# Kernel tuning notes

Measured on AMD Instinct MI355X. Metric: run time of the kernel, lower is better.

The kernel has to match this reference:

```python
import jax, jax.numpy as jnp
import numpy as np
from jax.scipy.ndimage import map_coordinates

B, H, W, C = 131072, 12, 12, 1

def setup_inputs() -> dict:
    key = jax.random.key(0)
    ks = jax.random.split(key, 9)
    s = 0.05
    return {
        "x":   jax.random.normal(ks[0], (B, H, W, C), jnp.float32),
        "k1":  jax.random.normal(ks[1], (7, 7, C, 8), jnp.float32) * s,
        "bc1": jnp.zeros((8,), jnp.float32),
        "k2":  jax.random.normal(ks[2], (5, 5, 8, 10), jnp.float32) * s,
        "bc2": jnp.zeros((10,), jnp.float32),
        "W1":  jax.random.normal(ks[3], (90, 32), jnp.float32) * s,
        "b1":  jnp.zeros((32,), jnp.float32),
        "W2":  jax.random.normal(ks[4], (32, 6), jnp.float32) * s,
        "b2":  jnp.array([1.0, 0.0, 0.0, 0.0, 1.0, 0.0], jnp.float32),  # near-identity transform
    }

def _conv(x, k, b):
    y = jax.lax.conv_general_dilated(x, k, window_strides=(1, 1), padding='SAME',
                                     dimension_numbers=('NHWC', 'HWIO', 'NHWC'))
    return y + b

def _maxpool2(x):
    return jax.lax.reduce_window(x, -jnp.inf, jax.lax.max,
                                 (1, 2, 2, 1), (1, 2, 2, 1), 'VALID')

def _forward(x, k1, bc1, k2, bc2, W1, b1, W2, b2):
    # localization network
    xs = jax.nn.relu(_maxpool2(_conv(x, k1, bc1)))     # (B,6,6,8)
    xs = jax.nn.relu(_maxpool2(_conv(xs, k2, bc2)))    # (B,3,3,10)
    b = x.shape[0]
    xs = xs.reshape(b, 90)
    theta = jax.nn.relu(xs @ W1 + b1) @ W2 + b2        # (B,6)
    # grid = inv((1+1e-5)*I2) @ theta  ==  theta / (1+1e-5)
    theta = (theta / (1.0 + 1e-5)).reshape(b, 2, 3)
    h, w = x.shape[1], x.shape[2]
    # target grid in normalized [-1,1] coords
    yn, xn = jnp.meshgrid(jnp.linspace(-1.0, 1.0, h), jnp.linspace(-1.0, 1.0, w), indexing='ij')
    tgt = jnp.stack([xn, yn, jnp.ones_like(xn)], 0).reshape(3, -1)  # (3, H*W)
    src = jnp.einsum('bij,jk->bik', theta, tgt)        # (B,2,H*W): (x_src, y_src)
    px = (src[:, 0] + 1.0) * (w - 1) * 0.5             # pixel coords
    py = (src[:, 1] + 1.0) * (h - 1) * 0.5
    coords = jnp.stack([py.reshape(b, h, w), px.reshape(b, h, w)], 1)  # (B,2,H,W)
    def sample_one(img, coord):  # img (H,W,C), coord (2,H,W)
        return jax.vmap(
            lambda ch: map_coordinates(ch, [coord[0], coord[1]], order=1, mode='reflect'),
            in_axes=2, out_axes=2)(img)
    return jax.vmap(sample_one)(x, coords)             # (B,H,W,C)

def reference(x, k1, bc1, k2, bc2, W1, b1, W2, b2):
    return _forward(x, k1, bc1, k2, bc2, W1, b1, W2, b2)
```

## Files before the change

### kernel.cpp

```cpp
#include <hip/hip_runtime.h>

typedef __attribute__((ext_vector_type(8))) short bfrag;
typedef __attribute__((ext_vector_type(4))) float facc;

__device__ __forceinline__ short f2bf(float f) {
    unsigned u = __float_as_uint(f);
    u += 0x7FFFu + ((u >> 16) & 1u);
    return (short)(u >> 16);
}
__device__ __forceinline__ int refl12(int i) {
    int r = i % 24; if (r < 0) r += 24; return (r < 12) ? r : 23 - r;
}
__device__ __forceinline__ facc mfma16(bfrag a, bfrag b, facc c) {
    return __builtin_amdgcn_mfma_f32_16x16x32_bf16(a, b, c, 0, 0, 0);
}

#define WB1_E 0
#define WB2_E 184320
#define W1T_E 350208
#define W2T_E 353280

#define XS1_STRIDE 296

__global__ void k0_build(const float* __restrict__ k1w, const float* __restrict__ k2w,
                         const float* __restrict__ W1, const float* __restrict__ W2,
                         short* __restrict__ ws)
{
    const int NW1 = 1152 * 160, NW2 = 576 * 288, NT1 = 32 * 96, NT2 = 16 * 32;
    const int total = NW1 + NW2 + NT1 + NT2;
    for (int q = blockIdx.x * blockDim.x + threadIdx.x; q < total;
         q += gridDim.x * blockDim.x) {
        float val = 0.f;
        short* dst;
        if (q < NW1) {
            int n = q / 160, kk = q - n * 160;
            dst = ws + WB1_E + q;
            int p1 = n >> 5, r = n & 31;
            int hy = (r >> 4) & 1, hx = (r >> 3) & 1, c = r & 7;
            int yp = p1 / 6, xp = p1 - yp * 6;
            int y = 2 * yp + hy, xo = 2 * xp + hx;
            if (kk < 144) {
                int yi = kk / 12, xi = kk - yi * 12;
                int ky = yi - y + 3, kx = xi - xo + 3;
                if (ky >= 0 && ky < 7 && kx >= 0 && kx < 7)
                    val = k1w[(ky * 7 + kx) * 8 + c];
            }
        } else if (q < NW1 + NW2) {
            int qq = q - NW1;
            int n = qq / 288, k2 = qq - n * 288;
            dst = ws + WB2_E + qq;
            int q2 = n >> 6, r = n & 63, g = r >> 4, c2 = r & 15;
            int gy = g >> 1, gx = g & 1;
            int qy = q2 / 3, qx = q2 - qy * 3;
            int Y = 2 * qy + gy, X = 2 * qx + gx;
            int p1 = k2 >> 3, c1 = k2 & 7;
            int yp = p1 / 6, xp = p1 - yp * 6;
            int ky = yp - Y + 2, kx = xp - X + 2;
            if (c2 < 10 && ky >= 0 && ky < 5 && kx >= 0 && kx < 5)
                val = k2w[((ky * 5 + kx) * 8 + c1) * 10 + c2];
        } else if (q < NW1 + NW2 + NT1) {
            int qq = q - NW1 - NW2;
            int j = qq / 96, k = qq - j * 96;
            dst = ws + W1T_E + qq;
            if (k < 90) val = W1[k * 32 + j];
        } else {
            int qq = q - NW1 - NW2 - NT1;
            int t = qq / 32, k = qq - t * 32;
            dst = ws + W2T_E + qq;
            if (t < 6) val = W2[k * 6 + t];
        }
        *dst = f2bf(val);
    }
}

__global__ __launch_bounds__(512) void k12_gemm(
    const float* __restrict__ x, const short* __restrict__ wb1,
    const short* __restrict__ wb2, const short* __restrict__ w1t,
    const short* __restrict__ w2t, const float* __restrict__ bc1,
    const float* __restrict__ bc2, const float* __restrict__ b1,
    const float* __restrict__ b2, float* __restrict__ theta, int B)
{
    __shared__ short xs1L[128 * XS1_STRIDE];
    __shared__ short XS2[128 * 128];
    __shared__ short FC1[128 * 64];

    const int tid = threadIdx.x;
    const int l = tid & 63, w = tid >> 6;
    const int mg = w >> 2, ng = w & 3;
    const int lr = l & 15, lg = l >> 4;
    const long long blkbase = (long long)blockIdx.x * 128;
    const int mloc = mg * 64;

    for (int q = tid; q < 2048; q += 512) {
        bfrag z = {0, 0, 0, 0, 0, 0, 0, 0};
        *(bfrag*)&XS2[q * 8] = z;
    }

    bfrag a[4][5];
    #pragma unroll
    for (int ms = 0; ms < 4; ++ms) {
        long long img = blkbase + mloc + ms * 16 + lr;
        if (img >= B) img = B - 1;
        const float* row = x + (size_t)img * 144;
        #pragma unroll
        for (int t = 0; t < 5; ++t) {
            const int k = t * 32 + lg * 8;
            bfrag f = {0, 0, 0, 0, 0, 0, 0, 0};
            if (k < 144) {
                float4 u0 = *(const float4*)(row + k);
                float4 u1 = *(const float4*)(row + k + 4);
                f[0] = f2bf(u0.x); f[1] = f2bf(u0.y);
                f[2] = f2bf(u0.z); f[3] = f2bf(u0.w);
                f[4] = f2bf(u1.x); f[5] = f2bf(u1.y);
                f[6] = f2bf(u1.z); f[7] = f2bf(u1.w);
            }
            a[ms][t] = f;
        }
    }
    const float bcv = bc1[l & 7];

    auto loadB1 = [&](bfrag (&bb)[2][5], int p1v) {
        const short* p = wb1 + (size_t)(p1v * 32 + lr) * 160 + lg * 8;
        #pragma unroll
        for (int nt = 0; nt < 2; ++nt)
            #pragma unroll
            for (int t = 0; t < 5; ++t)
                bb[nt][t] = *(const bfrag*)(p + (size_t)nt * 16 * 160 + t * 32);
    };
    auto compute1 = [&](bfrag (&bb)[2][5], int p1v) {
        facc acc[4][2];
        #pragma unroll
        for (int ms = 0; ms < 4; ++ms)
            #pragma unroll
            for (int nt = 0; nt < 2; ++nt)
                acc[ms][nt] = (facc){0.f, 0.f, 0.f, 0.f};
        #pragma unroll
        for (int t = 0; t < 5; ++t)
            #pragma unroll
            for (int nt = 0; nt < 2; ++nt)
                #pragma unroll
                for (int ms = 0; ms < 4; ++ms)
                    acc[ms][nt] = mfma16(a[ms][t], bb[nt][t], acc[ms][nt]);
        #pragma unroll
        for (int ms = 0; ms < 4; ++ms)
            #pragma unroll
            for (int i = 0; i < 4; ++i) {
                float p = fmaxf(acc[ms][0][i], acc[ms][1][i]);
                p = fmaxf(p, __shfl_xor(p, 8));
                p = fmaxf(p + bcv, 0.f);
                if ((l & 15) < 8) {
                    int mi = mloc + ms * 16 + lg * 4 + i;
                    xs1L[mi * XS1_STRIDE + p1v * 8 + (l & 7)] = f2bf(p);
                }
            }
    };

    {
        bfrag c0[2][5], c1[2][5];
        loadB1(c0, ng);
        #pragma unroll 1
        for (int jp = 0; jp < 4; ++jp) {
            loadB1(c1, (2 * jp + 1) * 4 + ng);
            compute1(c0, (2 * jp) * 4 + ng);
            loadB1(c0, (2 * jp + 2) * 4 + ng);
            compute1(c1, (2 * jp + 1) * 4 + ng);
        }
        compute1(c0, 32 + ng);
    }
    __syncthreads();

    const int c2 = lr;
    const float bcv2 = (c2 < 10) ? bc2[c2] : 0.f;

    auto loadB2 = [&](bfrag (&bb)[4], int q2v, int tv) {
        #pragma unroll
        for (int g = 0; g < 4; ++g)
            bb[g] = *(const bfrag*)(
                wb2 + (size_t)(q2v * 64 + g * 16 + lr) * 288 + tv * 32 + lg * 8);
    };

    {
        const int q2 = w;
        facc acc[8][4];
        #pragma unroll
        for (int ms = 0; ms < 8; ++ms)
            #pragma unroll
            for (int g = 0; g < 4; ++g)
                acc[ms][g] = (facc){0.f, 0.f, 0.f, 0.f};

        auto mstep8 = [&](bfrag (&bb)[4], int tv) {
            bfrag av[8];
            #pragma unroll
            for (int ms = 0; ms < 8; ++ms) {
                int m = ms * 16 + lr;
                av[ms] = *(const bfrag*)&xs1L[m * XS1_STRIDE + tv * 32 + lg * 8];
            }
            __builtin_amdgcn_s_setprio(1);
            #pragma unroll
            for (int g = 0; g < 4; ++g)
                #pragma unroll
                for (int ms = 0; ms < 8; ++ms)
                    acc[ms][g] = mfma16(av[ms], bb[g], acc[ms][g]);
            __builtin_amdgcn_s_setprio(0);
        };

        bfrag d0[4], d1[4];
        loadB2(d0, q2, 0);
        #pragma unroll 1
        for (int tp = 0; tp < 4; ++tp) {
            loadB2(d1, q2, 2 * tp + 1);
            mstep8(d0, 2 * tp);
            loadB2(d0, q2, 2 * tp + 2);
            mstep8(d1, 2 * tp + 1);
        }
        mstep8(d0, 8);

        #pragma unroll
        for (int ms = 0; ms < 8; ++ms)
            #pragma unroll
            for (int i = 0; i < 4; ++i) {
                float v = fmaxf(fmaxf(acc[ms][0][i], acc[ms][1][i]),
                                fmaxf(acc[ms][2][i], acc[ms][3][i]));
                v = fmaxf(v + bcv2, 0.f);
                if (c2 < 10) {
                    int mi = ms * 16 + lg * 4 + i;
                    int k = q2 * 10 + c2;
                    XS2[mi * 128 + (((k >> 3) ^ (mi & 7)) << 3) + (k & 7)] = f2bf(v);
                }
            }
    }

    if (w < 2) {
        const int q2 = 8;
        const int mBase = w * 64;
        facc acc[4][4];
        #pragma unroll
        for (int ms = 0; ms < 4; ++ms)
            #pragma unroll
            for (int g = 0; g < 4; ++g)
                acc[ms][g] = (facc){0.f, 0.f, 0.f, 0.f};

        auto mstep4 = [&](bfrag (&bb)[4], int tv) {
            bfrag av[4];
            #pragma unroll
            for (int ms = 0; ms < 4; ++ms) {
                int m = mBase + ms * 16 + lr;
                av[ms] = *(const bfrag*)&xs1L[m * XS1_STRIDE + tv * 32 + lg * 8];
            }
            __builtin_amdgcn_s_setprio(1);
            #pragma unroll
            for (int g = 0; g < 4; ++g)
                #pragma unroll
                for (int ms = 0; ms < 4; ++ms)
                    acc[ms][g] = mfma16(av[ms], bb[g], acc[ms][g]);
            __builtin_amdgcn_s_setprio(0);
        };

        bfrag d0[4], d1[4];
        loadB2(d0, q2, 0);
        #pragma unroll 1
        for (int tp = 0; tp < 4; ++tp) {
            loadB2(d1, q2, 2 * tp + 1);
            mstep4(d0, 2 * tp);
            loadB2(d0, q2, 2 * tp + 2);
            mstep4(d1, 2 * tp + 1);
        }
        mstep4(d0, 8);

        #pragma unroll
        for (int ms = 0; ms < 4; ++ms)
            #pragma unroll
            for (int i = 0; i < 4; ++i) {
                float v = fmaxf(fmaxf(acc[ms][0][i], acc[ms][1][i]),
                                fmaxf(acc[ms][2][i], acc[ms][3][i]));
                v = fmaxf(v + bcv2, 0.f);
                if (c2 < 10) {
                    int mi = mBase + ms * 16 + lg * 4 + i;
                    int k = q2 * 10 + c2;
                    XS2[mi * 128 + (((k >> 3) ^ (mi & 7)) << 3) + (k & 7)] = f2bf(v);
                }
            }
    }
    __syncthreads();

    {
        const int mg2 = w >> 1, nt = w & 1;
        facc acc[2];
        acc[0] = (facc){0.f, 0.f, 0.f, 0.f};
        acc[1] = (facc){0.f, 0.f, 0.f, 0.f};
        #pragma unroll
        for (int t = 0; t < 3; ++t) {
            const bfrag bv = *(const bfrag*)(w1t + (size_t)(nt * 16 + lr) * 96 + t * 32 + lg * 8);
            #pragma unroll
            for (int ms = 0; ms < 2; ++ms) {
                int m = mg2 * 32 + ms * 16 + lr;
                bfrag av = *(const bfrag*)&XS2[m * 128 + (((t * 4 + lg) ^ (m & 7)) << 3)];
                acc[ms] = mfma16(av, bv, acc[ms]);
            }
        }
        const int jcol = nt * 16 + lr;
        const float bj = b1[jcol];
        #pragma unroll
        for (int ms = 0; ms < 2; ++ms)
            #pragma unroll
            for (int i = 0; i < 4; ++i) {
                float v = fmaxf(acc[ms][i] + bj, 0.f);
                int mi = mg2 * 32 + ms * 16 + lg * 4 + i;
                FC1[mi * 64 + (((jcol >> 3) ^ (mi & 7)) << 3) + (jcol & 7)] = f2bf(v);
            }
    }
    __syncthreads();

    if (w < 4) {
        facc acc[2];
        acc[0] = (facc){0.f, 0.f, 0.f, 0.f};
        acc[1] = (facc){0.f, 0.f, 0.f, 0.f};
        const bfrag bv = *(const bfrag*)(w2t + (size_t)lr * 32 + lg * 8);
        #pragma unroll
        for (int ms = 0; ms < 2; ++ms) {
            int m = w * 32 + ms * 16 + lr;
            bfrag av = *(const bfrag*)&FC1[m * 64 + ((lg ^ (m & 7)) << 3)];
            acc[ms] = mfma16(av, bv, acc[ms]);
        }
        if (lr < 6) {
            const float tb = b2[lr];
            const float inv = 1.0f / (1.0f + 1e-5f);
            #pragma unroll
            for (int ms = 0; ms < 2; ++ms)
                #pragma unroll
                for (int i = 0; i < 4; ++i) {
                    long long img = blkbase + w * 32 + ms * 16 + lg * 4 + i;
                    if (img < B) theta[img * 6 + lr] = (acc[ms][i] + tb) * inv;
                }
        }
    }
}

__global__ __launch_bounds__(256) void k3_sample(
    const float* __restrict__ x, const float* __restrict__ theta,
    float* __restrict__ out, int B)
{
    __shared__ float xL[64 * 145];
    __shared__ float thL[64 * 6];
    const int tid = threadIdx.x;
    const long long blkbase = (long long)blockIdx.x * 64;

    const float4* xg4 = (const float4*)(x + blkbase * 144);
    for (int q = tid; q < 2304; q += 256) {
        int il = q / 36, c4 = q - il * 36;
        float4 v = make_float4(0.f, 0.f, 0.f, 0.f);
        if (blkbase + il < B) v = xg4[(size_t)il * 36 + c4];
        *(float4*)&xL[il * 145 + c4 * 4] = v;
    }
    for (int q = tid; q < 384; q += 256) {
        long long idx = blkbase * 6 + q;
        if (idx < (long long)B * 6) thL[q] = theta[idx];
    }
    __syncthreads();

    const int il = tid >> 2, quad = tid & 3;
    const long long img = blkbase + il;
    if (img >= B) return;

    const float t0 = thL[il * 6 + 0];
    const float t1 = thL[il * 6 + 1];
    const float t2 = thL[il * 6 + 2];
    const float t3 = thL[il * 6 + 3];
    const float t4 = thL[il * 6 + 4];
    const float t5 = thL[il * 6 + 5];
    const float* xr = &xL[il * 145];
    const float step = 2.0f / 11.0f;
    const float t0s = t0 * 5.5f, t3s = t3 * 5.5f;

    float o[36];
    #pragma unroll
    for (int rr = 0; rr < 3; ++rr) {
        const int iy = quad * 3 + rr;
        const float yn = -1.0f + iy * step;
        const float cx = (t1 * yn + t2 + 1.0f) * 5.5f;
        const float cy = (t4 * yn + t5 + 1.0f) * 5.5f;
        #pragma unroll
        for (int jx = 0; jx < 12; ++jx) {
            const float xn = -1.0f + jx * step;
            const float px = fmaf(t0s, xn, cx);
            const float py = fmaf(t3s, xn, cy);
            const float fy = floorf(py), fx = floorf(px);
            const float wy = py - fy,    wx = px - fx;
            const int ly = (int)fy, lx = (int)fx;
            const int y0 = refl12(ly), y1 = refl12(ly + 1);
            const int x0 = refl12(lx), x1 = refl12(lx + 1);
            const float v00 = xr[y0 * 12 + x0];
            const float v01 = xr[y0 * 12 + x1];
            const float v10 = xr[y1 * 12 + x0];
            const float v11 = xr[y1 * 12 + x1];
            const float r0 = v00 + wx * (v01 - v00);
            const float r1 = v10 + wx * (v11 - v10);
            o[rr * 12 + jx] = r0 + wy * (r1 - r0);
        }
    }
    float* op = out + (size_t)img * 144 + quad * 36;
    #pragma unroll
    for (int k = 0; k < 9; ++k)
        *(float4*)(op + 4 * k) = make_float4(o[4*k], o[4*k+1], o[4*k+2], o[4*k+3]);
}

extern "C" void kernel_launch(void* const* d_in, const int* in_sizes, int n_in,
                              void* d_out, int out_size, void* d_ws, size_t ws_size,
                              hipStream_t stream)
{
    const float* x   = (const float*)d_in[0];
    const float* k1w = (const float*)d_in[1];
    const float* bc1 = (const float*)d_in[2];
    const float* k2w = (const float*)d_in[3];
    const float* bc2 = (const float*)d_in[4];
    const float* W1  = (const float*)d_in[5];
    const float* b1  = (const float*)d_in[6];
    const float* W2  = (const float*)d_in[7];
    const float* b2  = (const float*)d_in[8];
    float* out = (float*)d_out;
    const int B = in_sizes[0] / 144;

    short* ws = (short*)d_ws;
    short* wb1 = ws + WB1_E;
    short* wb2 = ws + WB2_E;
    short* w1t = ws + W1T_E;
    short* w2t = ws + W2T_E;
    float* theta = (float*)((char*)d_ws + 707584);

    hipLaunchKernelGGL(k0_build, dim3(512), dim3(256), 0, stream,
                       k1w, k2w, W1, W2, ws);

    const int nb = (B + 127) / 128;
    hipLaunchKernelGGL(k12_gemm, dim3(nb), dim3(512), 0, stream,
                       x, wb1, wb2, w1t, w2t, bc1, bc2, b1, b2, theta, B);

    const int nb3 = (int)((B + 63) / 64);
    hipLaunchKernelGGL(k3_sample, dim3(nb3), dim3(256), 0, stream,
                       x, theta, out, B);
}
```

Measured before the change: 180.6 us.

## Spread ninth conv2 pool-quadrant work across all waves and use DPP for pair max

The leftover conv2 output group (q2=8), previously computed only by waves 0-1 in a separate tail phase, is folded into the main conv2 loop. Each of the 8 waves now computes one 16-row slice of it alongside its own group. This removes the load imbalance where six waves idled during the tail. It costs extra registers for a second set of B fragments and accumulators. The cross-lane max in the conv1 epilogue also swaps __shfl_xor for a DPP row_shr-style update, avoiding the LDS-based shuffle.

Result: slower. 211.8 us (+17.2%).

```diff
diff --git a/kernel.cpp b/kernel.cpp
--- a/kernel.cpp
+++ b/kernel.cpp
@@ -7,6 +7,11 @@
     unsigned u = __float_as_uint(f);
     u += 0x7FFFu + ((u >> 16) & 1u);
     return (short)(u >> 16);
+}
+__device__ __forceinline__ float maxpair8(float p) {
+    int r = __builtin_amdgcn_update_dpp(0, __float_as_int(p),
+                                        0x128 , 0xf, 0xf, true);
+    return fmaxf(p, __int_as_float(r));
 }
 __device__ __forceinline__ int refl12(int i) {
     int r = i % 24; if (r < 0) r += 24; return (r < 12) ? r : 23 - r;
@@ -146,7 +151,7 @@
             #pragma unroll
             for (int i = 0; i < 4; ++i) {
                 float p = fmaxf(acc[ms][0][i], acc[ms][1][i]);
-                p = fmaxf(p, __shfl_xor(p, 8));
+                p = maxpair8(p);
                 p = fmaxf(p + bcv, 0.f);
                 if ((l & 15) < 8) {
                     int mi = mloc + ms * 16 + lg * 4 + i;
@@ -182,38 +187,46 @@
     {
         const int q2 = w;
         facc acc[8][4];
+        facc acc8[4];
         #pragma unroll
         for (int ms = 0; ms < 8; ++ms)
             #pragma unroll
             for (int g = 0; g < 4; ++g)
                 acc[ms][g] = (facc){0.f, 0.f, 0.f, 0.f};
-
-        auto mstep8 = [&](bfrag (&bb)[4], int tv) {
+        #pragma unroll
+        for (int g = 0; g < 4; ++g)
+            acc8[g] = (facc){0.f, 0.f, 0.f, 0.f};
+
+        auto mstep = [&](bfrag (&bb)[4], bfrag (&ee)[4], int tv) {
             bfrag av[8];
             #pragma unroll
             for (int ms = 0; ms < 8; ++ms) {
                 int m = ms * 16 + lr;
                 av[ms] = *(const bfrag*)&xs1L[m * XS1_STRIDE + tv * 32 + lg * 8];
             }
+            bfrag av8 = *(const bfrag*)&xs1L[(w * 16 + lr) * XS1_STRIDE + tv * 32 + lg * 8];
             __builtin_amdgcn_s_setprio(1);
             #pragma unroll
             for (int g = 0; g < 4; ++g)
                 #pragma unroll
                 for (int ms = 0; ms < 8; ++ms)
                     acc[ms][g] = mfma16(av[ms], bb[g], acc[ms][g]);
+            #pragma unroll
+            for (int g = 0; g < 4; ++g)
+                acc8[g] = mfma16(av8, ee[g], acc8[g]);
             __builtin_amdgcn_s_setprio(0);
         };
 
-        bfrag d0[4], d1[4];
-        loadB2(d0, q2, 0);
+        bfrag d0[4], d1[4], e0[4], e1[4];
+        loadB2(d0, q2, 0); loadB2(e0, 8, 0);
         #pragma unroll 1
         for (int tp = 0; tp < 4; ++tp) {
-            loadB2(d1, q2, 2 * tp + 1);
-            mstep8(d0, 2 * tp);
-            loadB2(d0, q2, 2 * tp + 2);
-            mstep8(d1, 2 * tp + 1);
-        }
-        mstep8(d0, 8);
+            loadB2(d1, q2, 2 * tp + 1); loadB2(e1, 8, 2 * tp + 1);
+            mstep(d0, e0, 2 * tp);
+            loadB2(d0, q2, 2 * tp + 2); loadB2(e0, 8, 2 * tp + 2);
+            mstep(d1, e1, 2 * tp + 1);
+        }
+        mstep(d0, e0, 8);
 
         #pragma unroll
         for (int ms = 0; ms < 8; ++ms)
@@ -228,58 +241,17 @@
                     XS2[mi * 128 + (((k >> 3) ^ (mi & 7)) << 3) + (k & 7)] = f2bf(v);
                 }
             }
-    }
-
-    if (w < 2) {
-        const int q2 = 8;
-        const int mBase = w * 64;
-        facc acc[4][4];
-        #pragma unroll
-        for (int ms = 0; ms < 4; ++ms)
-            #pragma unroll
-            for (int g = 0; g < 4; ++g)
-                acc[ms][g] = (facc){0.f, 0.f, 0.f, 0.f};
-
-        auto mstep4 = [&](bfrag (&bb)[4], int tv) {
-            bfrag av[4];
-            #pragma unroll
-            for (int ms = 0; ms < 4; ++ms) {
-                int m = mBase + ms * 16 + lr;
-                av[ms] = *(const bfrag*)&xs1L[m * XS1_STRIDE + tv * 32 + lg * 8];
-            }
-            __builtin_amdgcn_s_setprio(1);
-            #pragma unroll
-            for (int g = 0; g < 4; ++g)
-                #pragma unroll
-                for (int ms = 0; ms < 4; ++ms)
-                    acc[ms][g] = mfma16(av[ms], bb[g], acc[ms][g]);
-            __builtin_amdgcn_s_setprio(0);
-        };
-
-        bfrag d0[4], d1[4];
-        loadB2(d0, q2, 0);
-        #pragma unroll 1
-        for (int tp = 0; tp < 4; ++tp) {
-            loadB2(d1, q2, 2 * tp + 1);
-            mstep4(d0, 2 * tp);
-            loadB2(d0, q2, 2 * tp + 2);
-            mstep4(d1, 2 * tp + 1);
-        }
-        mstep4(d0, 8);
-
-        #pragma unroll
-        for (int ms = 0; ms < 4; ++ms)
-            #pragma unroll
-            for (int i = 0; i < 4; ++i) {
-                float v = fmaxf(fmaxf(acc[ms][0][i], acc[ms][1][i]),
-                                fmaxf(acc[ms][2][i], acc[ms][3][i]));
-                v = fmaxf(v + bcv2, 0.f);
-                if (c2 < 10) {
-                    int mi = mBase + ms * 16 + lg * 4 + i;
-                    int k = q2 * 10 + c2;
-                    XS2[mi * 128 + (((k >> 3) ^ (mi & 7)) << 3) + (k & 7)] = f2bf(v);
-                }
-            }
+        #pragma unroll
+        for (int i = 0; i < 4; ++i) {
+            float v = fmaxf(fmaxf(acc8[0][i], acc8[1][i]),
+                            fmaxf(acc8[2][i], acc8[3][i]));
+            v = fmaxf(v + bcv2, 0.f);
+            if (c2 < 10) {
+                int mi = w * 16 + lg * 4 + i;
+                int k = 80 + c2;
+                XS2[mi * 128 + (((k >> 3) ^ (mi & 7)) << 3) + (k & 7)] = f2bf(v);
+            }
+        }
     }
     __syncthreads();
 
```
